# Performance work log

Hardware: AMD Instinct MI355X
Metric: run time of the kernel (lower is better)

The kernel has to match this reference:

```python
import jax, jax.numpy as jnp
import numpy as np
import math

SCOPE = 27
RICKER_WIDTH = 4.0
DAMP = 0.12
IN_CHANNELS = 128
BATCH, H, W = 64, 64, 64


def _mexican_hat(scope, std, damping):
    # Ricker (mexican hat) wavelet sampled on integer grid centered at scope//2,
    # matching weight_initialization.mexican_hat(scope, std, damping).
    x = np.arange(scope, dtype=np.float32) - scope // 2
    a = 2.0 / (np.sqrt(3.0 * std) * np.pi ** 0.25)
    wavelet = a * (1.0 - (x / std) ** 2) * np.exp(-(x ** 2) / (2.0 * std ** 2))
    return (damping * wavelet).astype(np.float32)


def setup_inputs() -> dict:
    key = jax.random.key(0)
    activations = jax.random.normal(key, (BATCH, IN_CHANNELS, H, W), dtype=jnp.float32)
    inhibition_filter = jnp.asarray(_mexican_hat(SCOPE, RICKER_WIDTH, DAMP)).reshape(1, 1, SCOPE)
    return {"activations": activations, "inhibition_filter": inhibition_filter}


def reference(activations, inhibition_filter):
    # activations: (N, C, H, W); inhibition_filter: (1, 1, scope)
    C = activations.shape[1]
    scope = inhibition_filter.shape[-1]

    # pad_roll: zero-pad filter to length C, roll so center lands at index 0 side
    pad_left = (C - scope) // 2
    pad_right = C - scope - pad_left
    k = jnp.concatenate([
        jnp.zeros((pad_left,), dtype=inhibition_filter.dtype),
        inhibition_filter[0, 0],
        jnp.zeros((pad_right,), dtype=inhibition_filter.dtype),
    ])
    k = jnp.roll(k, C // 2 + 1)  # (C,)

    # kronecker delta along channels
    delta = jnp.zeros((C,), dtype=activations.dtype).at[0].set(1.0)

    # frequency-domain deconvolution along the channel axis
    Fk = jnp.fft.fft(delta - k)  # (C,) complex
    sig = jnp.transpose(activations, (0, 2, 3, 1))  # NCHW -> NHWC
    out = jnp.fft.ifft(jnp.fft.fft(sig, axis=-1) / Fk, axis=-1).real
    return jnp.transpose(out, (0, 3, 1, 2)).astype(activations.dtype)
```

## Files before the change

kernel.cpp:

```cpp
#include <hip/hip_runtime.h>


typedef short bf16x8 __attribute__((ext_vector_type(8)));
typedef float f32x4 __attribute__((ext_vector_type(4)));

#define MFMA16x16x32 __builtin_amdgcn_mfma_f32_16x16x32_bf16

__device__ __forceinline__ unsigned short f2bf(float f) {
  union { float f; unsigned u; } v; v.f = f;
  unsigned u = v.u;
  u += 0x7fffu + ((u >> 16) & 1u);
  return (unsigned short)(u >> 16);
}

__global__ void build_g(const float* __restrict__ filt, float* __restrict__ g) {
  __shared__ float ct[128], st[128], fr[128], fi[128];
  const int t = threadIdx.x;
  const float ang = (float)t * 0.049087385212340526f;
  float s, c;
  __sincosf(ang, &s, &c);
  ct[t] = c; st[t] = s;
  __syncthreads();

  float re = 1.f, im = 0.f;
  for (int tt = 0; tt < 27; ++tt) {
    const int j = (115 + tt) & 127;
    const int idx = (j * t) & 127;
    const float kv = filt[tt];
    re -= kv * ct[idx];
    im += kv * st[idx];
  }
  fr[t] = re; fi[t] = im;
  __syncthreads();

  float acc = 0.f;
  for (int m = 0; m < 128; ++m) {
    const int idx = (m * t) & 127;
    const float dr = fr[m], di = fi[m];
    acc += (ct[idx] * dr + st[idx] * di) / (dr * dr + di * di);
  }
  g[t] = acc * (1.0f / 128.0f);
}

__global__ __launch_bounds__(256, 4) void conv_inhib(
    const float* __restrict__ X, const float* __restrict__ gtab,
    float* __restrict__ Y) {
  const int tid = threadIdx.x;
  const int l = tid & 63;
  const int w = tid >> 6;
  const int lane15 = l & 15;
  const int quad = l >> 4;

  const int mtile = (blockIdx.x << 2) + w;
  const int sg = mtile << 4;
  const int img = sg >> 12;
  const int spos = sg & 4095;

  const float* Xn = X + (size_t)img * (128 * 4096) + spos + lane15;
  float* Yn = Y + (size_t)img * (128 * 4096) + spos + (quad << 2);

  bf16x8 gf[8];
#pragma unroll
  for (int d = 0; d < 8; ++d) {
    const int base = (d << 4) + lane15 - (quad << 3);
#pragma unroll
    for (int j = 0; j < 8; ++j) {
      gf[d][j] = (short)f2bf(gtab[(base - j) & 127]);
    }
  }

  f32x4 acc[8];
#pragma unroll
  for (int nt = 0; nt < 8; ++nt) acc[nt] = (f32x4){0.f, 0.f, 0.f, 0.f};

#pragma unroll
  for (int kt = 0; kt < 4; ++kt) {
    const float* Xk = Xn + (size_t)((kt << 5) + (quad << 3)) * 4096;
    float xa[8];
#pragma unroll
    for (int j = 0; j < 8; ++j) xa[j] = Xk[(size_t)j * 4096];
    bf16x8 af;
#pragma unroll
    for (int j = 0; j < 8; ++j) af[j] = (short)f2bf(xa[j]);
#pragma unroll
    for (int nt = 0; nt < 8; ++nt) {
      acc[nt] = MFMA16x16x32(af, gf[(nt - (kt << 1)) & 7], acc[nt], 0, 0, 0);
    }
  }

#pragma unroll
  for (int nt = 0; nt < 8; ++nt) {
    const int c = (nt << 4) + lane15;
    float4 v;
    v.x = acc[nt][0]; v.y = acc[nt][1]; v.z = acc[nt][2]; v.w = acc[nt][3];
    *(float4*)(Yn + (size_t)c * 4096) = v;
  }
}

extern "C" void kernel_launch(void* const* d_in, const int* in_sizes, int n_in,
                              void* d_out, int out_size, void* d_ws, size_t ws_size,
                              hipStream_t stream) {
  const float* act = (const float*)d_in[0];
  const float* filt = (const float*)d_in[1];
  float* out = (float*)d_out;
  float* g = (float*)d_ws;

  build_g<<<1, 128, 0, stream>>>(filt, g);
  conv_inhib<<<4096, 256, 0, stream>>>(act, g, out);
}
```

Baseline: 251.2 us.

## Stage activation tile in LDS via direct global-to-LDS 16-byte loads

Each block now copies a 128-channel by 64-position tile into shared memory using global_load_lds with 16-byte transfers, replacing per-lane scattered 4-byte global loads. The MFMA A-fragments are then read from LDS. The aim is wider, coalesced global reads and fewer load instructions. In exchange it uses 32KB of LDS per block, which may reduce occupancy, and drops the occupancy hint from launch bounds.

```diff
diff --git a/kernel.cpp b/kernel.cpp
--- a/kernel.cpp
+++ b/kernel.cpp
@@ -42,22 +42,38 @@
   g[t] = acc * (1.0f / 128.0f);
 }
 
-__global__ __launch_bounds__(256, 4) void conv_inhib(
+__global__ __launch_bounds__(256) void conv_inhib(
     const float* __restrict__ X, const float* __restrict__ gtab,
     float* __restrict__ Y) {
+  __shared__ __align__(16) float tile[128 * 64];
+
   const int tid = threadIdx.x;
   const int l = tid & 63;
   const int w = tid >> 6;
   const int lane15 = l & 15;
   const int quad = l >> 4;
 
-  const int mtile = (blockIdx.x << 2) + w;
-  const int sg = mtile << 4;
-  const int img = sg >> 12;
-  const int spos = sg & 4095;
+  const int bid = blockIdx.x;
+  const int img = bid >> 6;
+  const int s0 = (bid & 63) << 6;
 
-  const float* Xn = X + (size_t)img * (128 * 4096) + spos + lane15;
-  float* Yn = Y + (size_t)img * (128 * 4096) + spos + (quad << 2);
+  const float* Xn = X + (size_t)img * (128 * 4096);
+  float* Yn = Y + (size_t)img * (128 * 4096) + s0 + (w << 4) + (quad << 2);
+
+  {
+    const int rsub = l >> 4;
+    const int soff = (l & 15) << 2;
+#pragma unroll
+    for (int i = 0; i < 8; ++i) {
+      const int t = (w << 3) + i;
+      const int r = (t << 2) + rsub;
+      const float* src = Xn + (size_t)r * 4096 + s0 + soff;
+      float* dst = &tile[(t << 2) * 64];
+      __builtin_amdgcn_global_load_lds(
+          (const __attribute__((address_space(1))) void*)src,
+          (__attribute__((address_space(3))) void*)dst, 16, 0, 0);
+    }
+  }
 
   bf16x8 gf[8];
 #pragma unroll
@@ -69,19 +85,18 @@
     }
   }
 
+  __syncthreads();
+
   f32x4 acc[8];
 #pragma unroll
   for (int nt = 0; nt < 8; ++nt) acc[nt] = (f32x4){0.f, 0.f, 0.f, 0.f};
 
 #pragma unroll
   for (int kt = 0; kt < 4; ++kt) {
-    const float* Xk = Xn + (size_t)((kt << 5) + (quad << 3)) * 4096;
-    float xa[8];
-#pragma unroll
-    for (int j = 0; j < 8; ++j) xa[j] = Xk[(size_t)j * 4096];
+    const float* row = &tile[((kt << 5) + (quad << 3)) * 64 + (w << 4) + lane15];
     bf16x8 af;
 #pragma unroll
-    for (int j = 0; j < 8; ++j) af[j] = (short)f2bf(xa[j]);
+    for (int j = 0; j < 8; ++j) af[j] = (short)f2bf(row[j * 64]);
 #pragma unroll
     for (int nt = 0; nt < 8; ++nt) {
       acc[nt] = MFMA16x16x32(af, gf[(nt - (kt << 1)) & 7], acc[nt], 0, 0, 0);
```

New measurement: 248.6 us. About the same (-1.0%).
